# Performance work log

Hardware: AMD Instinct MI355X
Metric: run time of the kernel (lower is better)

## Reference

```python
import jax, jax.numpy as jnp
import numpy as np

B, T, D = 64, 512, 1024          # batch, time_steps (== seq_len), input_dim
ACT_DIM, UOUT, OUT = 1024, 1024, 512  # hidden size, unit_output_dim, output_dim


def setup_inputs() -> dict:
    key = jax.random.key(0)
    k0, k1, k2, k3 = jax.random.split(key, 4)
    s = 0.02  # small init so the linear recurrence stays numerically tame
    return {
        "X": jax.random.normal(k0, (B, T, D), jnp.float32),
        "Wax": jax.random.normal(k1, (ACT_DIM, D), jnp.float32) * s,
        "Waa": jax.random.normal(k2, (ACT_DIM, ACT_DIM), jnp.float32) * s,
        "ba": jnp.zeros((ACT_DIM,), jnp.float32),
        "Wy": jax.random.normal(k3, (UOUT, ACT_DIM), jnp.float32) * s,
        "by": jnp.zeros((UOUT,), jnp.float32),
    }


def reference(X, Wax, Waa, ba, Wy, by):
    # Shared-weight Elman RNN cell, act = acty = Identity (module defaults).
    # Input has no NaN padding -> non_padded_length == T, every step runs the cell.
    def step(a, x_t):
        a_new = x_t @ Wax.T + a @ Waa.T + ba   # [B, ACT_DIM]
        y = a_new @ Wy.T + by                  # [B, UOUT]
        return a_new, y

    a0 = jnp.zeros((X.shape[0], Waa.shape[0]), X.dtype)
    _, Y = jax.lax.scan(step, a0, jnp.swapaxes(X, 0, 1))  # Y: [T, B, UOUT]
    Y = jnp.swapaxes(Y, 0, 1)                              # [B, T, UOUT]
    # return_sequences=False: Y[:, non_padded_length-output_dim : non_padded_length]
    return Y[:, T - OUT:T, :]
```

## Files before the change

### kernel.cpp

```cpp
#include <hip/hip_runtime.h>
#include <hip/hip_bf16.h>
#include <stdint.h>
#include <stddef.h>

using bf16 = __hip_bfloat16;
typedef short s16x8 __attribute__((ext_vector_type(8)));
typedef float f32x4 __attribute__((ext_vector_type(4)));

#define MFMA16(a, b, c) __builtin_amdgcn_mfma_f32_16x16x32_bf16((a), (b), (c), 0, 0, 0)

typedef __attribute__((address_space(1))) void gvoid;
typedef __attribute__((address_space(3))) void lvoid;
#define GLL16(gp, lp) __builtin_amdgcn_global_load_lds((gvoid*)(void*)(gp), (lvoid*)(lp), 16, 0, 0)

__device__ __forceinline__ short f2bf(float x) {
    bf16 h = __float2bfloat16(x);
    return __builtin_bit_cast(short, h);
}

__global__ void cvt_bf16(const float* __restrict__ in, bf16* __restrict__ out, int n) {
    int i = (blockIdx.x * blockDim.x + threadIdx.x) * 4;
    if (i < n) {
        float4 v = *(const float4*)(in + i);
        out[i + 0] = __float2bfloat16(v.x);
        out[i + 1] = __float2bfloat16(v.y);
        out[i + 2] = __float2bfloat16(v.z);
        out[i + 3] = __float2bfloat16(v.w);
    }
}

__global__ void zero_bf16(bf16* __restrict__ p, int n) {
    int i = (blockIdx.x * blockDim.x + threadIdx.x) * 8;
    if (i < n) {
        s16x8 z = {0, 0, 0, 0, 0, 0, 0, 0};
        *(s16x8*)(p + i) = z;
    }
}

__global__ __launch_bounds__(256) void transpose_bf16(
    const bf16* __restrict__ in, bf16* __restrict__ out)
{
    __shared__ bf16 t[64][72];
    const int bx = blockIdx.x * 64, by = blockIdx.y * 64;
    const int tid = threadIdx.x;
#pragma unroll
    for (int i = 0; i < 2; ++i) {
        const int r = (tid >> 3) + i * 32, c = (tid & 7) * 8;
        *(s16x8*)&t[r][c] = *(const s16x8*)(in + (size_t)(bx + r) * 1024 + by + c);
    }
    __syncthreads();
#pragma unroll
    for (int i = 0; i < 2; ++i) {
        const int r = (tid >> 3) + i * 32, c = (tid & 7) * 8;
        s16x8 v;
#pragma unroll
        for (int k = 0; k < 8; ++k) v[k] = __builtin_bit_cast(short, t[c + k][r]);
        *(s16x8*)(out + (size_t)(by + r) * 1024 + bx + c) = v;
    }
}

template<bool A_F32, bool OUT_F32, int REMAP>
__global__ __launch_bounds__(512, 2) void gemm_bt256(
    const void* __restrict__ Ap, const bf16* __restrict__ Bt,
    const float* __restrict__ bias, void* __restrict__ Cp)
{
    __shared__ __align__(16) bf16 lA[2][256 * 64];
    __shared__ __align__(16) bf16 lB[2][256 * 64];

    const int tid  = threadIdx.x;
    const int lane = tid & 63, wv = tid >> 6;
    const int wm = wv >> 2, wn = wv & 3;
    const int quad = lane >> 4, l16 = lane & 15;

    const int lid = blockIdx.y * 128 + blockIdx.x;
    const int wid = (lid & 7) * 64 + (lid >> 3);
    const int m0 = (wid >> 2) * 256;
    const int n0 = (wid & 3) * 256;

    const int sr = lane >> 3;
    const int sc = ((lane & 7) ^ sr) * 8;
    const int ar = tid >> 1;
    const int ah = tid & 1;

    const float* Af = (const float*)Ap;
    const bf16*  Ab = (const bf16*)Ap;

    f32x4 acc[8][4] = {};
    float4 vr[4][2];

#define STAGE_B6(buf, ko) do { \
    _Pragma("unroll") \
    for (int qi = 0; qi < 4; ++qi) { \
        const int q = wv * 4 + qi; \
        GLL16(Bt + (size_t)(n0 + q * 8 + sr) * 1024 + (ko) + sc, (char*)lB[buf] + q * 1024); \
    } } while (0)
#define STAGE_A_BF6(buf, ko) do { \
    _Pragma("unroll") \
    for (int qi = 0; qi < 4; ++qi) { \
        const int q = wv * 4 + qi; \
        GLL16(Ab + (size_t)(m0 + q * 8 + sr) * 1024 + (ko) + sc, (char*)lA[buf] + q * 1024); \
    } } while (0)
#define LOAD_A_F326(ko) do { \
    _Pragma("unroll") \
    for (int i = 0; i < 4; ++i) { \
        const int c = ah * 4 + i; \
        const float* srcp = Af + (size_t)(m0 + ar) * 1024 + (ko) + c * 8; \
        vr[i][0] = *(const float4*)(srcp); \
        vr[i][1] = *(const float4*)(srcp + 4); \
    } } while (0)
#define WRITE_A_F326(buf) do { \
    _Pragma("unroll") \
    for (int i = 0; i < 4; ++i) { \
        const int c = ah * 4 + i; \
        s16x8 w; \
        w[0] = f2bf(vr[i][0].x); w[1] = f2bf(vr[i][0].y); w[2] = f2bf(vr[i][0].z); w[3] = f2bf(vr[i][0].w); \
        w[4] = f2bf(vr[i][1].x); w[5] = f2bf(vr[i][1].y); w[6] = f2bf(vr[i][1].z); w[7] = f2bf(vr[i][1].w); \
        *(s16x8*)((char*)lA[buf] + ar * 128 + ((c ^ (ar & 7)) << 4)) = w; \
    } } while (0)

    if constexpr (A_F32) { LOAD_A_F326(0); WRITE_A_F326(0); }
    else                 { STAGE_A_BF6(0, 0); }
    STAGE_B6(0, 0);
    __syncthreads();

    int cur = 0;
    for (int t = 0; t < 16; ++t) {
        const int nxt = cur ^ 1;
        if (t < 15) {
            const int ko = (t + 1) * 64;
            if constexpr (A_F32) LOAD_A_F326(ko);
            else                 STAGE_A_BF6(nxt, ko);
            STAGE_B6(nxt, ko);
        }
#pragma unroll
        for (int kc = 0; kc < 2; ++kc) {
            s16x8 af[8], bg[4];
#pragma unroll
            for (int mt = 0; mt < 8; ++mt) {
                const int r = 128 * wm + 16 * mt + l16;
                const int c = kc * 4 + quad;
                af[mt] = *(const s16x8*)((const char*)lA[cur] + r * 128 + ((c ^ (r & 7)) * 16));
            }
#pragma unroll
            for (int nt = 0; nt < 4; ++nt) {
                const int r = 64 * wn + 16 * nt + l16;
                const int c = kc * 4 + quad;
                bg[nt] = *(const s16x8*)((const char*)lB[cur] + r * 128 + ((c ^ (r & 7)) * 16));
            }
#pragma unroll
            for (int mt = 0; mt < 8; ++mt)
#pragma unroll
                for (int nt = 0; nt < 4; ++nt)
                    acc[mt][nt] = MFMA16(af[mt], bg[nt], acc[mt][nt]);
        }
        if constexpr (A_F32) { if (t < 15) WRITE_A_F326(nxt); }
        __syncthreads();
        cur = nxt;
    }
#undef STAGE_B6
#undef STAGE_A_BF6
#undef LOAD_A_F326
#undef WRITE_A_F326

    float bv[4];
#pragma unroll
    for (int nt = 0; nt < 4; ++nt)
        bv[nt] = bias[n0 + 64 * wn + 16 * nt + l16];

#pragma unroll
    for (int mt = 0; mt < 8; ++mt) {
#pragma unroll
        for (int r = 0; r < 4; ++r) {
            const int m = m0 + 128 * wm + 16 * mt + 4 * quad + r;
            int om = m;
            if constexpr (REMAP == 1)      om = ((m & 511) << 6) | (m >> 9);
            else if constexpr (REMAP == 2) om = ((m & 63) << 9) | (m >> 6);
#pragma unroll
            for (int nt = 0; nt < 4; ++nt) {
                const int n = n0 + 64 * wn + 16 * nt + l16;
                const float val = acc[mt][nt][r] + bv[nt];
                if constexpr (OUT_F32) ((float*)Cp)[(size_t)om * 1024 + n] = val;
                else ((bf16*)Cp)[(size_t)om * 1024 + n] = __float2bfloat16(val);
            }
        }
    }
}

__global__ __launch_bounds__(512, 2) void fixup_k256(
    const bf16* __restrict__ CIN, const bf16* __restrict__ PBase,
    bf16* __restrict__ UA)
{
    __shared__ __align__(16) bf16 lA[2][256 * 64];
    __shared__ __align__(16) bf16 lB[2][256 * 64];
    const int tid  = threadIdx.x;
    const int lane = tid & 63, wv = tid >> 6;
    const int wm = wv >> 2, wn = wv & 3;
    const int quad = lane >> 4, l16 = lane & 15;

    const int lid = blockIdx.y * 8 + blockIdx.x;
    const int wid = (lid & 7) * 4 + (lid >> 3);
    const int m0 = (wid >> 2) * 256;
    const int n0 = (wid & 3) * 256;

    const int j = blockIdx.z;
    const bf16* Bt = PBase + (size_t)j * 1048576;
    const int sr = lane >> 3;
    const int sc = ((lane & 7) ^ sr) * 8;

#define STAGE_AB6(buf, ko) do { \
    _Pragma("unroll") \
    for (int qi = 0; qi < 4; ++qi) { \
        const int q = wv * 4 + qi; \
        GLL16(CIN + (size_t)(m0 + q * 8 + sr) * 1024 + (ko) + sc, (char*)lA[buf] + q * 1024); \
        GLL16(Bt  + (size_t)(n0 + q * 8 + sr) * 1024 + (ko) + sc, (char*)lB[buf] + q * 1024); \
    } } while (0)

    f32x4 acc[8][4] = {};
    STAGE_AB6(0, 0);
    __syncthreads();
    int cur = 0;
    for (int t = 0; t < 16; ++t) {
        const int nxt = cur ^ 1;
        if (t < 15) STAGE_AB6(nxt, (t + 1) * 64);
#pragma unroll
        for (int kc = 0; kc < 2; ++kc) {
            s16x8 af[8], bg[4];
#pragma unroll
            for (int mt = 0; mt < 8; ++mt) {
                const int r = 128 * wm + 16 * mt + l16;
                const int c = kc * 4 + quad;
                af[mt] = *(const s16x8*)((const char*)lA[cur] + r * 128 + ((c ^ (r & 7)) * 16));
            }
#pragma unroll
            for (int nt = 0; nt < 4; ++nt) {
                const int r = 64 * wn + 16 * nt + l16;
                const int c = kc * 4 + quad;
                bg[nt] = *(const s16x8*)((const char*)lB[cur] + r * 128 + ((c ^ (r & 7)) * 16));
            }
#pragma unroll
            for (int mt = 0; mt < 8; ++mt)
#pragma unroll
                for (int nt = 0; nt < 4; ++nt)
                    acc[mt][nt] = MFMA16(af[mt], bg[nt], acc[mt][nt]);
        }
        __syncthreads();
        cur = nxt;
    }
#undef STAGE_AB6
#pragma unroll
    for (int mt = 0; mt < 8; ++mt)
#pragma unroll
        for (int r = 0; r < 4; ++r) {
            const int vm = m0 + 128 * wm + 16 * mt + 4 * quad + r;
            const size_t grow = (size_t)(((vm >> 6) * 16 + j) * 64 + (vm & 63));
#pragma unroll
            for (int nt = 0; nt < 4; ++nt) {
                const int n = n0 + 64 * wn + 16 * nt + l16;
                bf16* p = UA + grow * 1024 + n;
                *p = __float2bfloat16(acc[mt][nt][r] + __bfloat162float(*p));
            }
        }
}

__global__ __launch_bounds__(256) void powmul(
    const bf16* __restrict__ Abase, const bf16* __restrict__ Bt,
    bf16* __restrict__ Dbase)
{
    __shared__ __align__(16) bf16 lA[2][128 * 64];
    __shared__ __align__(16) bf16 lB[2][128 * 64];
    const int tid  = threadIdx.x;
    const int lane = tid & 63, wv = tid >> 6;
    const int wm = wv & 1, wn = wv >> 1;
    const int quad = lane >> 4, l16 = lane & 15;
    const int m0 = blockIdx.x * 128, n0 = blockIdx.y * 128;
    const bf16* A = Abase + (size_t)blockIdx.z * 1048576;
    bf16* D       = Dbase + (size_t)blockIdx.z * 1048576;
    const int sr = lane >> 3;
    const int sc = ((lane & 7) ^ sr) * 8;

#define STAGE_AB(buf, ko) do { \
    _Pragma("unroll") \
    for (int qi = 0; qi < 4; ++qi) { \
        const int q = wv * 4 + qi; \
        GLL16(A  + (size_t)(m0 + q * 8 + sr) * 1024 + (ko) + sc, (char*)lA[buf] + q * 1024); \
        GLL16(Bt + (size_t)(n0 + q * 8 + sr) * 1024 + (ko) + sc, (char*)lB[buf] + q * 1024); \
    } } while (0)

    f32x4 acc[4][4] = {};
    STAGE_AB(0, 0);
    __syncthreads();
    int cur = 0;
    for (int t = 0; t < 16; ++t) {
        const int nxt = cur ^ 1;
        if (t < 15) STAGE_AB(nxt, (t + 1) * 64);
#pragma unroll
        for (int kc = 0; kc < 2; ++kc) {
            s16x8 af[4], bg[4];
#pragma unroll
            for (int mt = 0; mt < 4; ++mt) {
                const int r = 64 * wm + 16 * mt + l16;
                const int c = kc * 4 + quad;
                af[mt] = *(const s16x8*)((const char*)lA[cur] + r * 128 + ((c ^ (r & 7)) * 16));
            }
#pragma unroll
            for (int nt = 0; nt < 4; ++nt) {
                const int r = 64 * wn + 16 * nt + l16;
                const int c = kc * 4 + quad;
                bg[nt] = *(const s16x8*)((const char*)lB[cur] + r * 128 + ((c ^ (r & 7)) * 16));
            }
#pragma unroll
            for (int mt = 0; mt < 4; ++mt)
#pragma unroll
                for (int nt = 0; nt < 4; ++nt)
                    acc[mt][nt] = MFMA16(af[mt], bg[nt], acc[mt][nt]);
        }
        __syncthreads();
        cur = nxt;
    }
#undef STAGE_AB
#pragma unroll
    for (int mt = 0; mt < 4; ++mt)
#pragma unroll
        for (int r = 0; r < 4; ++r) {
            const int m = m0 + 64 * wm + 16 * mt + 4 * quad + r;
#pragma unroll
            for (int nt = 0; nt < 4; ++nt) {
                const int n = n0 + 64 * wn + 16 * nt + l16;
                D[(size_t)m * 1024 + n] = __float2bfloat16(acc[mt][nt][r]);
            }
        }
}

__global__ __launch_bounds__(256) void local_step(
    const bf16* __restrict__ Bt, bf16* __restrict__ UA, int j)
{
    __shared__ __align__(16) bf16 lA[2][64 * 64];
    __shared__ __align__(16) bf16 lB[2][128 * 64];
    const int tid = threadIdx.x;
    const int lane = tid & 63, wv = tid >> 6;
    const int quad = lane >> 4, l16 = lane & 15;
    const int n0 = blockIdx.y * 128;
    const int t_ = blockIdx.x * 16 + j;
    const bf16* src = UA + (size_t)(t_ - 1) * 64 * 1024;
    bf16* dst       = UA + (size_t)t_ * 64 * 1024;
    const int sr = lane >> 3;
    const int sc = ((lane & 7) ^ sr) * 8;

#define STAGE_AB(buf, ko) do { \
    _Pragma("unroll") \
    for (int qi = 0; qi < 2; ++qi) { \
        const int q = wv * 2 + qi; \
        GLL16(src + (size_t)(q * 8 + sr) * 1024 + (ko) + sc, (char*)lA[buf] + q * 1024); \
    } \
    _Pragma("unroll") \
    for (int qi = 0; qi < 4; ++qi) { \
        const int q = wv * 4 + qi; \
        GLL16(Bt + (size_t)(n0 + q * 8 + sr) * 1024 + (ko) + sc, (char*)lB[buf] + q * 1024); \
    } } while (0)

    f32x4 acc[4][2] = {};
    STAGE_AB(0, 0);
    __syncthreads();
    int cur = 0;
    for (int t = 0; t < 16; ++t) {
        const int nxt = cur ^ 1;
        if (t < 15) STAGE_AB(nxt, (t + 1) * 64);
#pragma unroll
        for (int kc = 0; kc < 2; ++kc) {
            s16x8 af[4], bg[2];
#pragma unroll
            for (int mt = 0; mt < 4; ++mt) {
                const int r = 16 * mt + l16;
                const int c = kc * 4 + quad;
                af[mt] = *(const s16x8*)((const char*)lA[cur] + r * 128 + ((c ^ (r & 7)) * 16));
            }
#pragma unroll
            for (int nt = 0; nt < 2; ++nt) {
                const int r = 32 * wv + 16 * nt + l16;
                const int c = kc * 4 + quad;
                bg[nt] = *(const s16x8*)((const char*)lB[cur] + r * 128 + ((c ^ (r & 7)) * 16));
            }
#pragma unroll
            for (int mt = 0; mt < 4; ++mt)
#pragma unroll
                for (int nt = 0; nt < 2; ++nt)
                    acc[mt][nt] = MFMA16(af[mt], bg[nt], acc[mt][nt]);
        }
        __syncthreads();
        cur = nxt;
    }
#undef STAGE_AB
#pragma unroll
    for (int mt = 0; mt < 4; ++mt)
#pragma unroll
        for (int r = 0; r < 4; ++r) {
            const int b = 16 * mt + 4 * quad + r;
#pragma unroll
            for (int nt = 0; nt < 2; ++nt) {
                const int n = n0 + 32 * wv + 16 * nt + l16;
                bf16* p = dst + (size_t)b * 1024 + n;
                *p = __float2bfloat16(acc[mt][nt][r] + __bfloat162float(*p));
            }
        }
}

__global__ __launch_bounds__(64, 1) void carry_step(
    const bf16* __restrict__ P16, const bf16* __restrict__ lend,
    const bf16* __restrict__ src, bf16* __restrict__ dst)
{
    const int lane = threadIdx.x;
    const int quad = lane >> 4, l16 = lane & 15;
    const int bi = blockIdx.x & 3, nj = blockIdx.x >> 2;

    const bf16* arow = src + ((size_t)(16 * bi + l16)) * 1024;
    const bf16* wrow = P16 + ((size_t)(16 * nj + l16)) * 1024;

    const bf16* urow = lend + ((size_t)(16 * bi + 4 * quad)) * 1024 + 16 * nj + l16;
    f32x4 acc;
#pragma unroll
    for (int rr = 0; rr < 4; ++rr)
        acc[rr] = __bfloat162float(urow[(size_t)rr * 1024]);

    s16x8 av[32], wf[32];
#pragma unroll
    for (int kc = 0; kc < 32; ++kc) {
        av[kc] = *(const s16x8*)(arow + kc * 32 + quad * 8);
        wf[kc] = *(const s16x8*)(wrow + kc * 32 + quad * 8);
    }
#pragma unroll
    for (int kc = 0; kc < 32; ++kc)
        acc = MFMA16(av[kc], wf[kc], acc);

    bf16* drow = dst + ((size_t)(16 * bi + 4 * quad)) * 1024 + 16 * nj + l16;
#pragma unroll
    for (int rr = 0; rr < 4; ++rr)
        drow[(size_t)rr * 1024] = __float2bfloat16(acc[rr]);
}

extern "C" void kernel_launch(void* const* d_in, const int* in_sizes, int n_in,
                              void* d_out, int out_size, void* d_ws, size_t ws_size,
                              hipStream_t stream) {
    const float* X   = (const float*)d_in[0];
    const float* Wax = (const float*)d_in[1];
    const float* Waa = (const float*)d_in[2];
    const float* ba  = (const float*)d_in[3];
    const float* Wy  = (const float*)d_in[4];
    const float* by  = (const float*)d_in[5];

    char* ws = (char*)d_ws;
    bf16* UA   = (bf16*)ws;
    bf16* PB   = (bf16*)(ws + 67108864);
    bf16* Waxb = (bf16*)(ws + 100663296);
    bf16* Wyb  = (bf16*)(ws + 102760448);
    bf16* CIN  = (bf16*)(ws + 104857600);
    bf16* Tb   = CIN;
    const size_t MM = 1048576;

    const int NW = 1024 * 1024;
    cvt_bf16<<<dim3(NW / 1024), dim3(256), 0, stream>>>(Wax, Waxb, NW);
    cvt_bf16<<<dim3(NW / 1024), dim3(256), 0, stream>>>(Waa, PB,   NW);
    cvt_bf16<<<dim3(NW / 1024), dim3(256), 0, stream>>>(Wy,  Wyb,  NW);

    dim3 gridG(128, 4), blk2(512), blk(256);
    gemm_bt256<true, false, 1><<<gridG, blk2, 0, stream>>>(X, Waxb, ba, UA);

    transpose_bf16<<<dim3(16, 16), blk, 0, stream>>>(PB, Tb);
    powmul<<<dim3(8, 8, 1), blk, 0, stream>>>(PB, Tb, PB + 1 * MM);
    transpose_bf16<<<dim3(16, 16), blk, 0, stream>>>(PB + 1 * MM, Tb);
    powmul<<<dim3(8, 8, 2), blk, 0, stream>>>(PB, Tb, PB + 2 * MM);
    transpose_bf16<<<dim3(16, 16), blk, 0, stream>>>(PB + 3 * MM, Tb);
    powmul<<<dim3(8, 8, 4), blk, 0, stream>>>(PB, Tb, PB + 4 * MM);
    transpose_bf16<<<dim3(16, 16), blk, 0, stream>>>(PB + 7 * MM, Tb);
    powmul<<<dim3(8, 8, 8), blk, 0, stream>>>(PB, Tb, PB + 8 * MM);

    for (int j = 1; j < 16; ++j)
        local_step<<<dim3(32, 8), blk, 0, stream>>>(PB, UA, j);

    zero_bf16<<<dim3(32), dim3(256), 0, stream>>>(CIN, 65536);
    for (int c = 1; c < 32; ++c)
        carry_step<<<dim3(256), dim3(64), 0, stream>>>(
            PB + 15 * MM,
            UA  + (size_t)((c - 1) * 16 + 15) * 65536,
            CIN + (size_t)(c - 1) * 65536,
            CIN + (size_t)c * 65536);

    fixup_k256<<<dim3(8, 4, 16), blk2, 0, stream>>>(CIN, PB, UA);

    gemm_bt256<false, true, 2><<<gridG, blk2, 0, stream>>>(UA, Wyb, by, (float*)d_out);
}
```

Measured before the change: 874.3 us.

## Use 8-wave ping-pong scheduled K-loop for bf16 GEMM and fixup kernels

Replaces the simple double-buffered K-loop in the bf16-input GEMM (output projection) and the fixup GEMM with a finer-grained schedule. Each K step is split into four quadrant MFMA phases, with half-tile global-to-LDS loads interleaved between them. It adds explicit s_waitcnt vmcnt counts, raw s_barrier calls and s_setprio around the MFMA bursts, aiming to overlap memory traffic with matrix math. The fp32-input GEMM is split out into its own unchanged kernel. The risks are more barriers per step and hand-tuned waitcount correctness.

```diff
diff --git a/kernel.cpp b/kernel.cpp
--- a/kernel.cpp
+++ b/kernel.cpp
@@ -59,9 +59,88 @@
     }
 }
 
-template<bool A_F32, bool OUT_F32, int REMAP>
-__global__ __launch_bounds__(512, 2) void gemm_bt256(
-    const void* __restrict__ Ap, const bf16* __restrict__ Bt,
+#define G8_READ_AF(mh) do { _Pragma("unroll") \
+    for (int mt = 0; mt < 4; ++mt) { _Pragma("unroll") \
+        for (int kc = 0; kc < 2; ++kc) { \
+            const int r = 128 * wm + 16 * ((mh) * 4 + mt) + l16; \
+            const int c = kc * 4 + quad; \
+            af[mt][kc] = *(const s16x8*)((const char*)lA[curb] + r * 128 + ((c ^ (r & 7)) * 16)); \
+        } } } while (0)
+
+#define G8_READ_BG(nh) do { _Pragma("unroll") \
+    for (int nt = 0; nt < 2; ++nt) { _Pragma("unroll") \
+        for (int kc = 0; kc < 2; ++kc) { \
+            const int r = 64 * wn + 16 * ((nh) * 2 + nt) + l16; \
+            const int c = kc * 4 + quad; \
+            bg[nt][kc] = *(const s16x8*)((const char*)lB[curb] + r * 128 + ((c ^ (r & 7)) * 16)); \
+        } } } while (0)
+
+#define G8_MFMA_Q(mh, nh) do { \
+    __builtin_amdgcn_s_setprio(1); \
+    _Pragma("unroll") \
+    for (int mt = 0; mt < 4; ++mt) \
+        _Pragma("unroll") \
+        for (int nt = 0; nt < 2; ++nt) \
+            _Pragma("unroll") \
+            for (int kc = 0; kc < 2; ++kc) \
+                acc[(mh) * 4 + mt][(nh) * 2 + nt] = \
+                    MFMA16(af[mt][kc], bg[nt][kc], acc[(mh) * 4 + mt][(nh) * 2 + nt]); \
+    __builtin_amdgcn_s_setprio(0); \
+    } while (0)
+
+#define G8_STAGE_A(Asrc, buf, h, ko) do { _Pragma("unroll") \
+    for (int qi = 0; qi < 2; ++qi) { \
+        const int q = (h) * 16 + wv * 2 + qi; \
+        GLL16(Asrc + (size_t)(m0 + q * 8 + sr) * 1024 + (ko) + sc, (char*)lA[buf] + q * 1024); \
+    } } while (0)
+#define G8_STAGE_B(Bsrc, buf, h, ko) do { _Pragma("unroll") \
+    for (int qi = 0; qi < 2; ++qi) { \
+        const int q = (h) * 16 + wv * 2 + qi; \
+        GLL16(Bsrc + (size_t)(n0 + q * 8 + sr) * 1024 + (ko) + sc, (char*)lB[buf] + q * 1024); \
+    } } while (0)
+
+#define G8_KLOOP(Asrc, Bsrc) \
+     \
+    G8_STAGE_A(Asrc, 0, 0, 0);  G8_STAGE_A(Asrc, 0, 1, 0); \
+    G8_STAGE_B(Bsrc, 0, 0, 0);  G8_STAGE_B(Bsrc, 0, 1, 0); \
+    G8_STAGE_A(Asrc, 1, 0, 64); G8_STAGE_A(Asrc, 1, 1, 64); \
+    asm volatile("s_waitcnt vmcnt(4)" ::: "memory"); \
+    __builtin_amdgcn_s_barrier(); \
+    for (int k = 0; k < 16; ++k) { \
+        const int nxtb = curb ^ 1; \
+        const int ko1 = (k + 1) * 64, ko2 = (k + 2) * 64; \
+         \
+        G8_READ_AF(0); G8_READ_BG(0); \
+        if (k < 15) G8_STAGE_B(Bsrc, nxtb, 0, ko1); \
+        __builtin_amdgcn_s_barrier(); \
+        G8_MFMA_Q(0, 0); \
+        __builtin_amdgcn_s_barrier(); \
+         \
+        G8_READ_BG(1); \
+        if (k < 15) G8_STAGE_B(Bsrc, nxtb, 1, ko1); \
+        __builtin_amdgcn_s_barrier(); \
+        G8_MFMA_Q(0, 1); \
+        __builtin_amdgcn_s_barrier(); \
+         \
+        G8_READ_AF(1); \
+        if (k < 14) G8_STAGE_A(Asrc, curb, 0, ko2); \
+        __builtin_amdgcn_s_barrier(); \
+        G8_MFMA_Q(1, 1); \
+        __builtin_amdgcn_s_barrier(); \
+         \
+        G8_READ_BG(0); \
+        if (k < 14) G8_STAGE_A(Asrc, curb, 1, ko2); \
+        __builtin_amdgcn_s_barrier(); \
+        G8_MFMA_Q(1, 0); \
+        if (k < 14)       { asm volatile("s_waitcnt vmcnt(4)" ::: "memory"); } \
+        else if (k == 14) { asm volatile("s_waitcnt vmcnt(0)" ::: "memory"); } \
+        __builtin_amdgcn_s_barrier(); \
+        curb = nxtb; \
+    }
+
+template<bool OUT_F32, int REMAP>
+__global__ __launch_bounds__(512, 2) void gemm8(
+    const bf16* __restrict__ Ab, const bf16* __restrict__ Bt,
     const float* __restrict__ bias, void* __restrict__ Cp)
 {
     __shared__ __align__(16) bf16 lA[2][256 * 64];
@@ -79,11 +158,101 @@
 
     const int sr = lane >> 3;
     const int sc = ((lane & 7) ^ sr) * 8;
+
+    f32x4 acc[8][4] = {};
+    s16x8 af[4][2], bg[2][2];
+    int curb = 0;
+
+    G8_KLOOP(Ab, Bt)
+
+    float bv[4];
+#pragma unroll
+    for (int nt = 0; nt < 4; ++nt)
+        bv[nt] = bias[n0 + 64 * wn + 16 * nt + l16];
+
+#pragma unroll
+    for (int mt = 0; mt < 8; ++mt) {
+#pragma unroll
+        for (int r = 0; r < 4; ++r) {
+            const int m = m0 + 128 * wm + 16 * mt + 4 * quad + r;
+            int om = m;
+            if constexpr (REMAP == 1)      om = ((m & 511) << 6) | (m >> 9);
+            else if constexpr (REMAP == 2) om = ((m & 63) << 9) | (m >> 6);
+#pragma unroll
+            for (int nt = 0; nt < 4; ++nt) {
+                const int n = n0 + 64 * wn + 16 * nt + l16;
+                const float val = acc[mt][nt][r] + bv[nt];
+                if constexpr (OUT_F32) ((float*)Cp)[(size_t)om * 1024 + n] = val;
+                else ((bf16*)Cp)[(size_t)om * 1024 + n] = __float2bfloat16(val);
+            }
+        }
+    }
+}
+
+__global__ __launch_bounds__(512, 2) void fixup8(
+    const bf16* __restrict__ CIN, const bf16* __restrict__ PBase,
+    bf16* __restrict__ UA)
+{
+    __shared__ __align__(16) bf16 lA[2][256 * 64];
+    __shared__ __align__(16) bf16 lB[2][256 * 64];
+
+    const int tid  = threadIdx.x;
+    const int lane = tid & 63, wv = tid >> 6;
+    const int wm = wv >> 2, wn = wv & 3;
+    const int quad = lane >> 4, l16 = lane & 15;
+
+    const int lid = blockIdx.y * 8 + blockIdx.x;
+    const int wid = (lid & 7) * 4 + (lid >> 3);
+    const int m0 = (wid >> 2) * 256;
+    const int n0 = (wid & 3) * 256;
+
+    const int j = blockIdx.z;
+    const bf16* Bt = PBase + (size_t)j * 1048576;
+    const int sr = lane >> 3;
+    const int sc = ((lane & 7) ^ sr) * 8;
+
+    f32x4 acc[8][4] = {};
+    s16x8 af[4][2], bg[2][2];
+    int curb = 0;
+
+    G8_KLOOP(CIN, Bt)
+
+#pragma unroll
+    for (int mt = 0; mt < 8; ++mt)
+#pragma unroll
+        for (int r = 0; r < 4; ++r) {
+            const int vm = m0 + 128 * wm + 16 * mt + 4 * quad + r;
+            const size_t grow = (size_t)(((vm >> 6) * 16 + j) * 64 + (vm & 63));
+#pragma unroll
+            for (int nt = 0; nt < 4; ++nt) {
+                const int n = n0 + 64 * wn + 16 * nt + l16;
+                bf16* p = UA + grow * 1024 + n;
+                *p = __float2bfloat16(acc[mt][nt][r] + __bfloat162float(*p));
+            }
+        }
+}
+
+__global__ __launch_bounds__(512, 2) void gemm_bt256_af32(
+    const float* __restrict__ Af, const bf16* __restrict__ Bt,
+    const float* __restrict__ bias, bf16* __restrict__ Cp)
+{
+    __shared__ __align__(16) bf16 lA[2][256 * 64];
+    __shared__ __align__(16) bf16 lB[2][256 * 64];
+
+    const int tid  = threadIdx.x;
+    const int lane = tid & 63, wv = tid >> 6;
+    const int wm = wv >> 2, wn = wv & 3;
+    const int quad = lane >> 4, l16 = lane & 15;
+
+    const int lid = blockIdx.y * 128 + blockIdx.x;
+    const int wid = (lid & 7) * 64 + (lid >> 3);
+    const int m0 = (wid >> 2) * 256;
+    const int n0 = (wid & 3) * 256;
+
+    const int sr = lane >> 3;
+    const int sc = ((lane & 7) ^ sr) * 8;
     const int ar = tid >> 1;
     const int ah = tid & 1;
-
-    const float* Af = (const float*)Ap;
-    const bf16*  Ab = (const bf16*)Ap;
 
     f32x4 acc[8][4] = {};
     float4 vr[4][2];
@@ -93,12 +262,6 @@
     for (int qi = 0; qi < 4; ++qi) { \
         const int q = wv * 4 + qi; \
         GLL16(Bt + (size_t)(n0 + q * 8 + sr) * 1024 + (ko) + sc, (char*)lB[buf] + q * 1024); \
-    } } while (0)
-#define STAGE_A_BF6(buf, ko) do { \
-    _Pragma("unroll") \
-    for (int qi = 0; qi < 4; ++qi) { \
-        const int q = wv * 4 + qi; \
-        GLL16(Ab + (size_t)(m0 + q * 8 + sr) * 1024 + (ko) + sc, (char*)lA[buf] + q * 1024); \
     } } while (0)
 #define LOAD_A_F326(ko) do { \
     _Pragma("unroll") \
@@ -118,8 +281,7 @@
         *(s16x8*)((char*)lA[buf] + ar * 128 + ((c ^ (ar & 7)) << 4)) = w; \
     } } while (0)
 
-    if constexpr (A_F32) { LOAD_A_F326(0); WRITE_A_F326(0); }
-    else                 { STAGE_A_BF6(0, 0); }
+    LOAD_A_F326(0); WRITE_A_F326(0);
     STAGE_B6(0, 0);
     __syncthreads();
 
@@ -127,14 +289,12 @@
     for (int t = 0; t < 16; ++t) {
         const int nxt = cur ^ 1;
         if (t < 15) {
-            const int ko = (t + 1) * 64;
-            if constexpr (A_F32) LOAD_A_F326(ko);
-            else                 STAGE_A_BF6(nxt, ko);
-            STAGE_B6(nxt, ko);
+            LOAD_A_F326((t + 1) * 64);
+            STAGE_B6(nxt, (t + 1) * 64);
         }
 #pragma unroll
         for (int kc = 0; kc < 2; ++kc) {
-            s16x8 af[8], bg[4];
+            s16x8 af[8], bgv[4];
 #pragma unroll
             for (int mt = 0; mt < 8; ++mt) {
                 const int r = 128 * wm + 16 * mt + l16;
@@ -145,20 +305,19 @@
             for (int nt = 0; nt < 4; ++nt) {
                 const int r = 64 * wn + 16 * nt + l16;
                 const int c = kc * 4 + quad;
-                bg[nt] = *(const s16x8*)((const char*)lB[cur] + r * 128 + ((c ^ (r & 7)) * 16));
+                bgv[nt] = *(const s16x8*)((const char*)lB[cur] + r * 128 + ((c ^ (r & 7)) * 16));
             }
 #pragma unroll
             for (int mt = 0; mt < 8; ++mt)
 #pragma unroll
                 for (int nt = 0; nt < 4; ++nt)
-                    acc[mt][nt] = MFMA16(af[mt], bg[nt], acc[mt][nt]);
-        }
-        if constexpr (A_F32) { if (t < 15) WRITE_A_F326(nxt); }
+                    acc[mt][nt] = MFMA16(af[mt], bgv[nt], acc[mt][nt]);
+        }
+        if (t < 15) WRITE_A_F326(nxt);
         __syncthreads();
         cur = nxt;
     }
 #undef STAGE_B6
-#undef STAGE_A_BF6
 #undef LOAD_A_F326
 #undef WRITE_A_F326
 
@@ -172,94 +331,14 @@
 #pragma unroll
         for (int r = 0; r < 4; ++r) {
             const int m = m0 + 128 * wm + 16 * mt + 4 * quad + r;
-            int om = m;
-            if constexpr (REMAP == 1)      om = ((m & 511) << 6) | (m >> 9);
-            else if constexpr (REMAP == 2) om = ((m & 63) << 9) | (m >> 6);
+            const int om = ((m & 511) << 6) | (m >> 9);
 #pragma unroll
             for (int nt = 0; nt < 4; ++nt) {
                 const int n = n0 + 64 * wn + 16 * nt + l16;
-                const float val = acc[mt][nt][r] + bv[nt];
-                if constexpr (OUT_F32) ((float*)Cp)[(size_t)om * 1024 + n] = val;
-                else ((bf16*)Cp)[(size_t)om * 1024 + n] = __float2bfloat16(val);
-            }
-        }
-    }
-}
-
-__global__ __launch_bounds__(512, 2) void fixup_k256(
-    const bf16* __restrict__ CIN, const bf16* __restrict__ PBase,
-    bf16* __restrict__ UA)
-{
-    __shared__ __align__(16) bf16 lA[2][256 * 64];
-    __shared__ __align__(16) bf16 lB[2][256 * 64];
-    const int tid  = threadIdx.x;
-    const int lane = tid & 63, wv = tid >> 6;
-    const int wm = wv >> 2, wn = wv & 3;
-    const int quad = lane >> 4, l16 = lane & 15;
-
-    const int lid = blockIdx.y * 8 + blockIdx.x;
-    const int wid = (lid & 7) * 4 + (lid >> 3);
-    const int m0 = (wid >> 2) * 256;
-    const int n0 = (wid & 3) * 256;
-
-    const int j = blockIdx.z;
-    const bf16* Bt = PBase + (size_t)j * 1048576;
-    const int sr = lane >> 3;
-    const int sc = ((lane & 7) ^ sr) * 8;
-
-#define STAGE_AB6(buf, ko) do { \
-    _Pragma("unroll") \
-    for (int qi = 0; qi < 4; ++qi) { \
-        const int q = wv * 4 + qi; \
-        GLL16(CIN + (size_t)(m0 + q * 8 + sr) * 1024 + (ko) + sc, (char*)lA[buf] + q * 1024); \
-        GLL16(Bt  + (size_t)(n0 + q * 8 + sr) * 1024 + (ko) + sc, (char*)lB[buf] + q * 1024); \
-    } } while (0)
-
-    f32x4 acc[8][4] = {};
-    STAGE_AB6(0, 0);
-    __syncthreads();
-    int cur = 0;
-    for (int t = 0; t < 16; ++t) {
-        const int nxt = cur ^ 1;
-        if (t < 15) STAGE_AB6(nxt, (t + 1) * 64);
-#pragma unroll
-        for (int kc = 0; kc < 2; ++kc) {
-            s16x8 af[8], bg[4];
-#pragma unroll
-            for (int mt = 0; mt < 8; ++mt) {
-                const int r = 128 * wm + 16 * mt + l16;
-                const int c = kc * 4 + quad;
-                af[mt] = *(const s16x8*)((const char*)lA[cur] + r * 128 + ((c ^ (r & 7)) * 16));
-            }
-#pragma unroll
-            for (int nt = 0; nt < 4; ++nt) {
-                const int r = 64 * wn + 16 * nt + l16;
-                const int c = kc * 4 + quad;
-                bg[nt] = *(const s16x8*)((const char*)lB[cur] + r * 128 + ((c ^ (r & 7)) * 16));
-            }
-#pragma unroll
-            for (int mt = 0; mt < 8; ++mt)
-#pragma unroll
-                for (int nt = 0; nt < 4; ++nt)
-                    acc[mt][nt] = MFMA16(af[mt], bg[nt], acc[mt][nt]);
-        }
-        __syncthreads();
-        cur = nxt;
-    }
-#undef STAGE_AB6
-#pragma unroll
-    for (int mt = 0; mt < 8; ++mt)
-#pragma unroll
-        for (int r = 0; r < 4; ++r) {
-            const int vm = m0 + 128 * wm + 16 * mt + 4 * quad + r;
-            const size_t grow = (size_t)(((vm >> 6) * 16 + j) * 64 + (vm & 63));
-#pragma unroll
-            for (int nt = 0; nt < 4; ++nt) {
-                const int n = n0 + 64 * wn + 16 * nt + l16;
-                bf16* p = UA + grow * 1024 + n;
-                *p = __float2bfloat16(acc[mt][nt][r] + __bfloat162float(*p));
-            }
-        }
+                Cp[(size_t)om * 1024 + n] = __float2bfloat16(acc[mt][nt][r] + bv[nt]);
+            }
+        }
+    }
 }
 
 __global__ __launch_bounds__(256) void powmul(
@@ -462,7 +541,7 @@
     cvt_bf16<<<dim3(NW / 1024), dim3(256), 0, stream>>>(Wy,  Wyb,  NW);
 
     dim3 gridG(128, 4), blk2(512), blk(256);
-    gemm_bt256<true, false, 1><<<gridG, blk2, 0, stream>>>(X, Waxb, ba, UA);
+    gemm_bt256_af32<<<gridG, blk2, 0, stream>>>(X, Waxb, ba, UA);
 
     transpose_bf16<<<dim3(16, 16), blk, 0, stream>>>(PB, Tb);
     powmul<<<dim3(8, 8, 1), blk, 0, stream>>>(PB, Tb, PB + 1 * MM);
@@ -484,7 +563,7 @@
             CIN + (size_t)(c - 1) * 65536,
             CIN + (size_t)c * 65536);
 
-    fixup_k256<<<dim3(8, 4, 16), blk2, 0, stream>>>(CIN, PB, UA);
-
-    gemm_bt256<false, true, 2><<<gridG, blk2, 0, stream>>>(UA, Wyb, by, (float*)d_out);
-}
+    fixup8<<<dim3(8, 4, 16), blk2, 0, stream>>>(CIN, PB, UA);
+
+    gemm8<true, 2><<<gridG, blk2, 0, stream>>>(UA, Wyb, by, (float*)d_out);
+}
```

Result: no change. 866.9 us (-0.8%).
